# Performance work log

Measured on AMD Instinct MI355X. Metric: run time of the kernel, lower is better.

## Reference

```python
import jax, jax.numpy as jnp
import numpy as np

BATCH, SEQ, DIM = 4, 4096, 2048
NUM_EXPERTS, TOP_K, RANK = 8, 2, 16
SCALING = 1.0


def setup_inputs() -> dict:
    key = jax.random.key(0)
    k0, k1, k2, k3 = jax.random.split(key, 4)
    s = 0.02
    x = jax.random.normal(k0, (BATCH, SEQ, DIM), dtype=jnp.float32)
    gate_W = jax.random.normal(k1, (NUM_EXPERTS, DIM), dtype=jnp.float32) * s  # [E, D] torch Linear layout
    gate_b = jnp.zeros((NUM_EXPERTS,), dtype=jnp.float32)
    A = jax.random.normal(k2, (NUM_EXPERTS, RANK, DIM), dtype=jnp.float32) * s   # lora_A weights [E, R, D]
    Bm = jax.random.normal(k3, (NUM_EXPERTS, DIM, RANK), dtype=jnp.float32) * s  # lora_B weights [E, D, R]
    return {"x": x, "gate_W": gate_W, "gate_b": gate_b, "A": A, "Bm": Bm}


def reference(x, gate_W, gate_b, A, Bm):
    # Gate: logits [B, S, E], softmax probs
    logits = jnp.einsum('bsd,ed->bse', x, gate_W) + gate_b
    gate_probs = jax.nn.softmax(logits, axis=-1)
    # Top-k selection. NOTE: the original torch code computes topk weights but
    # NEVER uses them -- expert outputs are summed unweighted over the top-k set.
    _, idx = jax.lax.top_k(gate_probs, TOP_K)  # idx: [B, S, K]
    # mask[b,s,e] = expert e is in token (b,s)'s top-k
    mask = jnp.any(idx[..., :, None] == jnp.arange(NUM_EXPERTS), axis=-2)  # [B, S, E] bool
    # Dense grouped LoRA: h [B, S, E, R] (small, rank=16), masked before combine
    h = jnp.einsum('bsd,erd->bser', x, A)
    h = jax.nn.gelu(h, approximate=False) * mask[..., None].astype(x.dtype)
    out = jnp.einsum('bser,edr->bsd', h, Bm) * SCALING  # [B, S, D]
    return out, gate_probs
```

## Files before the change

### kernel.cpp

```cpp
#include <hip/hip_runtime.h>
#include <math.h>

#define NTOK 16384
#define DIM  2048
#define NEXP 8
#define RANK 16

typedef unsigned short ushort_t;
typedef unsigned int   uint_t;
typedef __attribute__((ext_vector_type(8))) short bf16x8;
typedef __attribute__((ext_vector_type(4))) float f32x4;

__device__ __forceinline__ ushort_t f2bf(float f) {
  union { float f; uint_t u; } v; v.f = f;
  uint_t r = (v.u + 0x7FFFu + ((v.u >> 16) & 1u)) >> 16;
  return (ushort_t)r;
}
__device__ __forceinline__ float bf2f(ushort_t s) {
  union { uint_t u; float f; } v; v.u = ((uint_t)s) << 16;
  return v.f;
}

__device__ __forceinline__ void gl_lds16(const ushort_t* g, ushort_t* l) {
  __builtin_amdgcn_global_load_lds(
      (const __attribute__((address_space(1))) unsigned int*)g,
      (__attribute__((address_space(3))) unsigned int*)l, 16, 0, 0);
}

__global__ __launch_bounds__(256) void k0_prep(
    const float* __restrict__ gW, const float* __restrict__ A,
    const float* __restrict__ Bm,
    ushort_t* __restrict__ Wc, ushort_t* __restrict__ Bm2) {
  int b = blockIdx.x, t = threadIdx.x;
  if (b < 1280) {
    int idx = b * 256 + t;
    int r = idx >> 11, d = idx & 2047;
    float v;
    if (r < 8)        v = gW[r * 2048 + d];
    else if (r < 16)  v = 0.f;
    else if (r < 144) v = A[(size_t)(r - 16) * 2048 + d];
    else if (r < 152) { float g = gW[(r - 144) * 2048 + d]; v = g - bf2f(f2bf(g)); }
    else              v = 0.f;
    int ch = d >> 6, c = d & 63;
    int cs = ((((c >> 3) ^ (r & 7)) << 3) | (c & 7));
    Wc[((size_t)ch * 160 + r) * 64 + cs] = f2bf(v);
  } else {
    int idx = (b - 1280) * 256 + t;
    int dd = idx >> 7, c = idx & 127, e = c >> 4, rr = c & 15;
    Bm2[idx] = f2bf(Bm[((size_t)e * 2048 + dd) * 16 + rr]);
  }
}

#define BKP 72

__global__ __launch_bounds__(256) void k1_gate_h(
    const float* __restrict__ x, const float* __restrict__ gate_b,
    const ushort_t* __restrict__ Wc,
    ushort_t* __restrict__ Hm, float* __restrict__ probs) {
  __shared__ __align__(16) ushort_t ws_w[2][160 * 64];
  __shared__ __align__(16) ushort_t xs_hi[2][32][BKP];
  __shared__ __align__(16) ushort_t xs_lo[2][32][BKP];
  __shared__ float Cs[32][152];
  __shared__ int sel0s[32], sel1s[32];

  const int t = threadIdx.x;
  const int lane = t & 63, wave = t >> 6;
  const int l15 = lane & 15, q = lane >> 4;
  const int mt = wave & 1;
  const int ng = wave >> 1;
  const int ntiles = ng ? 5 : 4;
  const int tok0 = blockIdx.x * 32;

  f32x4 acc[5];
  #pragma unroll
  for (int i = 0; i < 5; ++i) acc[i] = (f32x4)0.f;

  const float4* xg = (const float4*)(x + (size_t)tok0 * DIM);
  const int xrow0 = t >> 4, xc4 = t & 15;

  float4 xv[2];

  auto load_x = [&](int ch) {
    xv[0] = xg[xrow0 * (DIM / 4) + ch * 16 + xc4];
    xv[1] = xg[(16 + xrow0) * (DIM / 4) + ch * 16 + xc4];
  };
  auto stage_w = [&](int ch, int buf) {
    const ushort_t* src = Wc + (size_t)ch * (160 * 64);
    #pragma unroll
    for (int i = 0; i < 5; ++i)
      gl_lds16(src + (size_t)(i * 256 + t) * 8,
               &ws_w[buf][(i * 256 + wave * 64) * 8]);
  };
  auto write_x = [&](int buf) {
    #pragma unroll
    for (int i = 0; i < 2; ++i) {
      int row = xrow0 + i * 16;
      float vv[4] = {xv[i].x, xv[i].y, xv[i].z, xv[i].w};
      ushort_t h4[4], l4[4];
      #pragma unroll
      for (int j = 0; j < 4; ++j) {
        h4[j] = f2bf(vv[j]);
        l4[j] = f2bf(vv[j] - bf2f(h4[j]));
      }
      *(uint2*)&xs_hi[buf][row][xc4 * 4] = *(const uint2*)h4;
      *(uint2*)&xs_lo[buf][row][xc4 * 4] = *(const uint2*)l4;
    }
  };

  load_x(0);
  stage_w(0, 0);
  write_x(0);
  __syncthreads();

  for (int ch = 0; ch < 32; ++ch) {
    const int cur = ch & 1, nxt = cur ^ 1;
    if (ch < 31) { load_x(ch + 1); stage_w(ch + 1, nxt); }

    const ushort_t* wb = ws_w[cur];
    auto wfrag = [&](int r, int kkg) -> bf16x8 {
      int pos = (r << 3) + ((kkg + q) ^ (r & 7));
      return *(const bf16x8*)&wb[pos << 3];
    };

    #pragma unroll
    for (int kk = 0; kk < 64; kk += 32) {
      const int kkg = kk >> 3;
      bf16x8 ah = *(const bf16x8*)&xs_hi[cur][mt * 16 + l15][kk + q * 8];
      if (ng == 0) {
        bf16x8 al  = *(const bf16x8*)&xs_lo[cur][mt * 16 + l15][kk + q * 8];
        bf16x8 bgl = wfrag(144 + l15, kkg);
        bf16x8 b0  = wfrag(l15, kkg);
        acc[0] = __builtin_amdgcn_mfma_f32_16x16x32_bf16(ah, b0, acc[0], 0, 0, 0);
        acc[0] = __builtin_amdgcn_mfma_f32_16x16x32_bf16(al, b0, acc[0], 0, 0, 0);
        acc[0] = __builtin_amdgcn_mfma_f32_16x16x32_bf16(ah, bgl, acc[0], 0, 0, 0);
        #pragma unroll
        for (int nt = 1; nt < 4; ++nt) {
          bf16x8 b = wfrag(nt * 16 + l15, kkg);
          acc[nt] = __builtin_amdgcn_mfma_f32_16x16x32_bf16(ah, b, acc[nt], 0, 0, 0);
        }
      } else {
        #pragma unroll
        for (int nt = 0; nt < 5; ++nt) {
          bf16x8 b = wfrag(64 + nt * 16 + l15, kkg);
          acc[nt] = __builtin_amdgcn_mfma_f32_16x16x32_bf16(ah, b, acc[nt], 0, 0, 0);
        }
      }
    }

    if (ch < 31) write_x(nxt);
    __syncthreads();
  }

  const int colbase = ng ? 64 : 0;
  #pragma unroll
  for (int i = 0; i < 5; ++i) {
    if (i < ntiles) {
      #pragma unroll
      for (int r = 0; r < 4; ++r)
        Cs[mt * 16 + q * 4 + r][colbase + i * 16 + l15] = acc[i][r];
    }
  }
  __syncthreads();

  if (t < 32) {
    int m = t;
    float lg[NEXP];
    #pragma unroll
    for (int e = 0; e < NEXP; ++e) lg[e] = Cs[m][e] + gate_b[e];
    float mx = lg[0];
    #pragma unroll
    for (int e = 1; e < NEXP; ++e) mx = fmaxf(mx, lg[e]);
    float ex[NEXP], s = 0.f;
    #pragma unroll
    for (int e = 0; e < NEXP; ++e) { ex[e] = __expf(lg[e] - mx); s += ex[e]; }
    float inv = 1.f / s;
    float4 p0 = make_float4(ex[0] * inv, ex[1] * inv, ex[2] * inv, ex[3] * inv);
    float4 p1 = make_float4(ex[4] * inv, ex[5] * inv, ex[6] * inv, ex[7] * inv);
    float* pp = probs + (size_t)(tok0 + m) * NEXP;
    *(float4*)pp = p0; *(float4*)(pp + 4) = p1;
    int i0 = 0;
    #pragma unroll
    for (int e = 1; e < NEXP; ++e) if (lg[e] > lg[i0]) i0 = e;
    int i1 = (i0 == 0) ? 1 : 0;
    #pragma unroll
    for (int e = 0; e < NEXP; ++e) if (e != i0 && lg[e] > lg[i1]) i1 = e;
    sel0s[m] = i0; sel1s[m] = i1;
  }
  __syncthreads();

  {
    int m = t >> 3, e = t & 7;
    int on = (e == sel0s[m]) | (e == sel1s[m]);
    ushort_t ov[16];
    #pragma unroll
    for (int r = 0; r < RANK; ++r) {
      float v = Cs[m][16 + e * 16 + r];
      float g = on ? (0.5f * v * (1.f + erff(v * 0.70710678118654752f))) : 0.f;
      ov[r] = f2bf(g);
    }
    ushort_t* hp = Hm + ((size_t)(tok0 + m) * 128 + e * 16);
    *(uint4*)hp       = *(const uint4*)&ov[0];
    *(uint4*)(hp + 8) = *(const uint4*)&ov[8];
  }
}

__global__ __launch_bounds__(64) void k2_combine(
    const ushort_t* __restrict__ Hm, const ushort_t* __restrict__ Bm2,
    float* __restrict__ out) {
  const int lane = threadIdx.x;
  const int l15 = lane & 15, q = lane >> 4;
  const int t0 = blockIdx.x * 32;
  const int nb = blockIdx.y * 256;

  bf16x8 a[2][4];
  #pragma unroll
  for (int mt = 0; mt < 2; ++mt)
    #pragma unroll
    for (int kk = 0; kk < 4; ++kk)
      a[mt][kk] = *(const bf16x8*)&Hm[(size_t)(t0 + mt * 16 + l15) * 128 + kk * 32 + q * 8];

  const ushort_t* bp = Bm2 + (size_t)(nb + l15) * 128 + q * 8;

  auto loadB = [&](bf16x8* dst, int i) {
    #pragma unroll
    for (int k = 0; k < 4; ++k)
      dst[k] = *(const bf16x8*)(bp + (size_t)i * 2048 + k * 32);
  };
  auto comp = [&](const bf16x8* bb, int i) {
    #pragma unroll
    for (int mt = 0; mt < 2; ++mt) {
      f32x4 c = (f32x4)0.f;
      #pragma unroll
      for (int k = 0; k < 4; ++k)
        c = __builtin_amdgcn_mfma_f32_16x16x32_bf16(a[mt][k], bb[k], c, 0, 0, 0);
      #pragma unroll
      for (int r = 0; r < 4; ++r)
        out[(size_t)(t0 + mt * 16 + q * 4 + r) * DIM + nb + i * 16 + l15] = c[r];
    }
  };

  bf16x8 bA[4], bB[4];
  loadB(bA, 0);
  #pragma unroll
  for (int ii = 0; ii < 8; ++ii) {
    loadB(bB, 2 * ii + 1);
    comp(bA, 2 * ii);
    if (ii < 7) loadB(bA, 2 * ii + 2);
    comp(bB, 2 * ii + 1);
  }
}

extern "C" void kernel_launch(void* const* d_in, const int* in_sizes, int n_in,
                              void* d_out, int out_size, void* d_ws, size_t ws_size,
                              hipStream_t stream) {
  const float* x      = (const float*)d_in[0];
  const float* gate_W = (const float*)d_in[1];
  const float* gate_b = (const float*)d_in[2];
  const float* A      = (const float*)d_in[3];
  const float* Bm     = (const float*)d_in[4];

  float* out   = (float*)d_out;
  float* probs = out + (size_t)NTOK * DIM;

  ushort_t* Wc  = (ushort_t*)d_ws;
  ushort_t* Bm2 = Wc + 32 * 160 * 64;
  ushort_t* Hm  = Bm2 + 2048 * 128;

  k0_prep<<<dim3(2304), dim3(256), 0, stream>>>(gate_W, A, Bm, Wc, Bm2);
  k1_gate_h<<<dim3(NTOK / 32), dim3(256), 0, stream>>>(x, gate_b, Wc, Hm, probs);
  k2_combine<<<dim3(NTOK / 32, DIM / 256), dim3(64), 0, stream>>>(Hm, Bm2, out);
}
```

Baseline: 314.5 us.

## Fuse LoRA combine into gate/h kernel, keeping H in LDS

Merges the combine GEMM into the gate/projection kernel. The bf16 H tile is written into reused LDS (XOR-swizzled) instead of global memory, and each of the four waves computes a 512-column slice of the output for the block's 32 tokens. The MFMA operands are swapped so each lane writes a contiguous float4 of output. This removes one launch and the H round trip to global memory, but the combine phase now runs on only 512 blocks with 4 waves each and sits serially after the gate phase, which may reduce parallelism during the output-write-bound stage.

```diff
diff --git a/kernel.cpp b/kernel.cpp
--- a/kernel.cpp
+++ b/kernel.cpp
@@ -53,15 +53,16 @@
 
 #define BKP 72
 
-__global__ __launch_bounds__(256) void k1_gate_h(
+__global__ __launch_bounds__(256) void k1_fused(
     const float* __restrict__ x, const float* __restrict__ gate_b,
-    const ushort_t* __restrict__ Wc,
-    ushort_t* __restrict__ Hm, float* __restrict__ probs) {
+    const ushort_t* __restrict__ Wc, const ushort_t* __restrict__ Bm2,
+    float* __restrict__ out, float* __restrict__ probs) {
   __shared__ __align__(16) ushort_t ws_w[2][160 * 64];
   __shared__ __align__(16) ushort_t xs_hi[2][32][BKP];
   __shared__ __align__(16) ushort_t xs_lo[2][32][BKP];
   __shared__ float Cs[32][152];
   __shared__ int sel0s[32], sel1s[32];
+  ushort_t* hm_s = &ws_w[0][0];
 
   const int t = threadIdx.x;
   const int lane = t & 63, wave = t >> 6;
@@ -198,55 +199,50 @@
       float g = on ? (0.5f * v * (1.f + erff(v * 0.70710678118654752f))) : 0.f;
       ov[r] = f2bf(g);
     }
-    ushort_t* hp = Hm + ((size_t)(tok0 + m) * 128 + e * 16);
-    *(uint4*)hp       = *(const uint4*)&ov[0];
-    *(uint4*)(hp + 8) = *(const uint4*)&ov[8];
-  }
-}
-
-__global__ __launch_bounds__(64) void k2_combine(
-    const ushort_t* __restrict__ Hm, const ushort_t* __restrict__ Bm2,
-    float* __restrict__ out) {
-  const int lane = threadIdx.x;
-  const int l15 = lane & 15, q = lane >> 4;
-  const int t0 = blockIdx.x * 32;
-  const int nb = blockIdx.y * 256;
-
-  bf16x8 a[2][4];
-  #pragma unroll
-  for (int mt = 0; mt < 2; ++mt)
-    #pragma unroll
-    for (int kk = 0; kk < 4; ++kk)
-      a[mt][kk] = *(const bf16x8*)&Hm[(size_t)(t0 + mt * 16 + l15) * 128 + kk * 32 + q * 8];
-
-  const ushort_t* bp = Bm2 + (size_t)(nb + l15) * 128 + q * 8;
-
-  auto loadB = [&](bf16x8* dst, int i) {
-    #pragma unroll
-    for (int k = 0; k < 4; ++k)
-      dst[k] = *(const bf16x8*)(bp + (size_t)i * 2048 + k * 32);
-  };
-  auto comp = [&](const bf16x8* bb, int i) {
-    #pragma unroll
-    for (int mt = 0; mt < 2; ++mt) {
-      f32x4 c = (f32x4)0.f;
+    int g0 = (2 * e) ^ (m & 7), g1 = (2 * e + 1) ^ (m & 7);
+    *(uint4*)&hm_s[m * 128 + g0 * 8] = *(const uint4*)&ov[0];
+    *(uint4*)&hm_s[m * 128 + g1 * 8] = *(const uint4*)&ov[8];
+  }
+  __syncthreads();
+
+  {
+    bf16x8 af[2][4];
+    #pragma unroll
+    for (int m2 = 0; m2 < 2; ++m2) {
+      int tok = m2 * 16 + l15;
+      #pragma unroll
+      for (int kk = 0; kk < 4; ++kk)
+        af[m2][kk] = *(const bf16x8*)&hm_s[tok * 128 + (((kk * 4 + q) ^ (tok & 7)) << 3)];
+    }
+
+    const int ncol0 = wave * 512;
+    const ushort_t* bp = Bm2 + (size_t)(ncol0 + l15) * 128 + q * 8;
+
+    auto loadB = [&](bf16x8* dst, int i) {
       #pragma unroll
       for (int k = 0; k < 4; ++k)
-        c = __builtin_amdgcn_mfma_f32_16x16x32_bf16(a[mt][k], bb[k], c, 0, 0, 0);
-      #pragma unroll
-      for (int r = 0; r < 4; ++r)
-        out[(size_t)(t0 + mt * 16 + q * 4 + r) * DIM + nb + i * 16 + l15] = c[r];
-    }
-  };
-
-  bf16x8 bA[4], bB[4];
-  loadB(bA, 0);
-  #pragma unroll
-  for (int ii = 0; ii < 8; ++ii) {
-    loadB(bB, 2 * ii + 1);
-    comp(bA, 2 * ii);
-    if (ii < 7) loadB(bA, 2 * ii + 2);
-    comp(bB, 2 * ii + 1);
+        dst[k] = *(const bf16x8*)(bp + (size_t)i * 2048 + k * 32);
+    };
+    auto comp = [&](const bf16x8* bb, int i) {
+      #pragma unroll
+      for (int m2 = 0; m2 < 2; ++m2) {
+        f32x4 c = (f32x4)0.f;
+        #pragma unroll
+        for (int k = 0; k < 4; ++k)
+          c = __builtin_amdgcn_mfma_f32_16x16x32_bf16(bb[k], af[m2][k], c, 0, 0, 0);
+        *(f32x4*)&out[(size_t)(tok0 + m2 * 16 + l15) * DIM + ncol0 + i * 16 + q * 4] = c;
+      }
+    };
+
+    bf16x8 bA[4], bB[4];
+    loadB(bA, 0);
+    #pragma unroll
+    for (int ii = 0; ii < 16; ++ii) {
+      loadB(bB, 2 * ii + 1);
+      comp(bA, 2 * ii);
+      if (ii < 15) loadB(bA, 2 * ii + 2);
+      comp(bB, 2 * ii + 1);
+    }
   }
 }
 
@@ -264,9 +260,7 @@
 
   ushort_t* Wc  = (ushort_t*)d_ws;
   ushort_t* Bm2 = Wc + 32 * 160 * 64;
-  ushort_t* Hm  = Bm2 + 2048 * 128;
 
   k0_prep<<<dim3(2304), dim3(256), 0, stream>>>(gate_W, A, Bm, Wc, Bm2);
-  k1_gate_h<<<dim3(NTOK / 32), dim3(256), 0, stream>>>(x, gate_b, Wc, Hm, probs);
-  k2_combine<<<dim3(NTOK / 32, DIM / 256), dim3(64), 0, stream>>>(Hm, Bm2, out);
-}
+  k1_fused<<<dim3(NTOK / 32), dim3(256), 0, stream>>>(x, gate_b, Wc, Bm2, out, probs);
+}
```

Measured after the change: 275.9 us. 1.14x faster.
